# Optimization experiments

Hardware: AMD Instinct MI355X
Metric: run time of the kernel (lower is better)

## Reference

```python
import jax, jax.numpy as jnp
import numpy as np

C = 64            # in_channels
IC = C // 2       # inter_channels (channel_rate=2)
R = 16            # reduction_ratio
EPS = 1e-5


def setup_inputs() -> dict:
    key = jax.random.key(0)
    ks = jax.random.split(key, 16)
    s = 0.05
    return {
        "x": jax.random.normal(ks[0], (16, C, 64, 25), dtype=jnp.float32),
        # 1x1 conv projections (common_v, key, query): [out, in] + bias
        "Wv": jax.random.normal(ks[1], (IC, C), dtype=jnp.float32) * s,
        "bv": jax.random.normal(ks[2], (IC,), dtype=jnp.float32) * s,
        "Wk": jax.random.normal(ks[3], (IC, C), dtype=jnp.float32) * s,
        "bk": jax.random.normal(ks[4], (IC,), dtype=jnp.float32) * s,
        "Wq": jax.random.normal(ks[5], (IC, C), dtype=jnp.float32) * s,
        "bq": jax.random.normal(ks[6], (IC,), dtype=jnp.float32) * s,
        # Trans_s: conv1x1 back to C + BatchNorm2d params (nonzero so output is non-trivial)
        "Wt": jax.random.normal(ks[7], (C, IC), dtype=jnp.float32) * s,
        "bt": jax.random.normal(ks[8], (C,), dtype=jnp.float32) * s,
        "gamma": jax.random.normal(ks[9], (C,), dtype=jnp.float32) * 0.5 + 1.0,
        "beta": jax.random.normal(ks[10], (C,), dtype=jnp.float32) * s,
        # ChannelGate MLP: Linear(C, C//R), Linear(C//R, C)
        "W1": jax.random.normal(ks[11], (C // R, C), dtype=jnp.float32) * s,
        "b1": jax.random.normal(ks[12], (C // R,), dtype=jnp.float32) * s,
        "W2": jax.random.normal(ks[13], (C, C // R), dtype=jnp.float32) * s,
        "b2": jax.random.normal(ks[14], (C,), dtype=jnp.float32) * s,
    }


def _conv1x1(x, W, b):
    # x: [N, Cin, T, V]; W: [Cout, Cin]
    return jnp.einsum('nctv,oc->notv', x, W) + b[None, :, None, None]


def reference(x, Wv, bv, Wk, bk, Wq, bq, Wt, bt, gamma, beta, W1, b1, W2, b2):
    N, Cc, T, V = x.shape
    TV = T * V
    ic = Wv.shape[0]

    v_x = _conv1x1(x, Wv, bv).reshape(N, ic, TV).transpose(0, 2, 1)  # [N, TV, ic]
    k_x = _conv1x1(x, Wk, bk).reshape(N, ic, TV).transpose(0, 2, 1)  # [N, TV, ic]
    q_x = _conv1x1(x, Wq, bq).reshape(N, ic, TV)                      # [N, ic, TV]

    # Unscaled dot-product attention over TV tokens (full [N, TV, TV] matrix)
    A = jnp.einsum('nti,nis->nts', k_x, q_x)
    attn = jax.nn.softmax(A, axis=-1)
    p = jnp.einsum('nts,nsi->nti', attn, v_x)                         # [N, TV, ic]
    p = p.transpose(0, 2, 1).reshape(N, ic, T, V)

    # Trans_s: conv1x1 + BatchNorm2d (training-mode batch statistics)
    p = _conv1x1(p, Wt, bt)
    mean = p.mean(axis=(0, 2, 3), keepdims=True)
    var = p.var(axis=(0, 2, 3), keepdims=True)
    p = (p - mean) * jax.lax.rsqrt(var + EPS)
    p = p * gamma[None, :, None, None] + beta[None, :, None, None]

    # ChannelGate (avg pool only) applied to original x
    avg = x.mean(axis=(2, 3))                                          # [N, C]
    h = jax.nn.relu(avg @ W1.T + b1)
    gate = jax.nn.sigmoid(h @ W2.T + b2)                               # [N, C]

    return gate[:, :, None, None] * p + x
```

## Files before the change

kernel.cpp:

```cpp
#include <hip/hip_runtime.h>
#include <hip/hip_bf16.h>
#include <math.h>

#define NB   16
#define CC   64
#define ICH  32
#define TV   1600
#define NTV  (NB*TV)

typedef __bf16 bf16x8 __attribute__((ext_vector_type(8)));
typedef float  f32x4  __attribute__((ext_vector_type(4)));

__global__ __launch_bounds__(256) void proj_gate_kernel(
    const float* __restrict__ x,
    const float* __restrict__ Wv, const float* __restrict__ bv,
    const float* __restrict__ Wk, const float* __restrict__ bk,
    const float* __restrict__ Wq, const float* __restrict__ bq,
    __bf16* __restrict__ Qb, __bf16* __restrict__ Kb,
    __bf16* __restrict__ VTb, float* __restrict__ AVG) {
  if (blockIdx.x >= 400) {
    int b = blockIdx.x - 400;
    int n = b >> 2, cq = b & 3;
    int c16 = threadIdx.x >> 4, l = threadIdx.x & 15;
    int c = cq * 16 + c16;
    const float4* xp = (const float4*)(x + ((size_t)n * CC + c) * TV) + l;
    float s = 0.f;
#pragma unroll
    for (int i = 0; i < 25; ++i) {
      float4 v = xp[i * 16];
      s += v.x + v.y + v.z + v.w;
    }
#pragma unroll
    for (int off = 8; off >= 1; off >>= 1) s += __shfl_down(s, off, 16);
    if (l == 0) AVG[n * CC + c] = s * (1.0f / (float)TV);
    return;
  }

  int tile = blockIdx.x >> 2;
  int og   = blockIdx.x & 3;
  int ob = og * 8;
  int tvIdx = tile * 256 + threadIdx.x;
  int n = tvIdx / TV, tv = tvIdx % TV;

  float av[8], ak[8], aq[8];
#pragma unroll
  for (int j = 0; j < 8; ++j) { av[j] = bv[ob+j]; ak[j] = bk[ob+j]; aq[j] = bq[ob+j]; }

  const float* xp = x + (size_t)n * CC * TV + tv;
#pragma unroll 8
  for (int c = 0; c < CC; ++c) {
    float xc = xp[c * TV];
#pragma unroll
    for (int j = 0; j < 8; ++j) {
      av[j] = fmaf(Wv[(ob + j) * CC + c], xc, av[j]);
      ak[j] = fmaf(Wk[(ob + j) * CC + c], xc, ak[j]);
      aq[j] = fmaf(Wq[(ob + j) * CC + c], xc, aq[j]);
    }
  }

  bf16x8 t;
#pragma unroll
  for (int j = 0; j < 8; ++j) t[j] = (__bf16)ak[j];
  int base = (n * TV + tv) * ICH + ob;
  *(bf16x8*)(Qb + base) = t;
#pragma unroll
  for (int j = 0; j < 8; ++j) t[j] = (__bf16)aq[j];
  *(bf16x8*)(Kb + base) = t;
#pragma unroll
  for (int j = 0; j < 8; ++j)
    VTb[(n * ICH + ob + j) * TV + tv] = (__bf16)av[j];
}

__global__ __launch_bounds__(256) void attn_kernel(
    const __bf16* __restrict__ Qb, const __bf16* __restrict__ Kb,
    const __bf16* __restrict__ VTb, float* __restrict__ P) {
  __shared__ __bf16 lds[4 * 4608];
  int b = blockIdx.x;
  int r8 = b & 7, qq = b >> 3;
  int n = r8 * 2 + (qq >= 50 ? 1 : 0);
  int rowTile = (qq >= 50) ? qq - 50 : qq;
  int row0 = rowTile * 32;

  int w = threadIdx.x >> 6;
  int lane = threadIdx.x & 63;
  int m = lane & 15, q = lane >> 4;

  __bf16* Pw = lds + w * 4608;

  const __bf16* Qn = Qb  + (size_t)n * TV * ICH;
  const __bf16* Kn = Kb  + (size_t)n * TV * ICH;
  const __bf16* Vn = VTb + (size_t)n * ICH * TV;

  bf16x8 aQ0 = *(const bf16x8*)(Qn + (row0 + m) * ICH + q * 8);
  bf16x8 aQ1 = *(const bf16x8*)(Qn + (row0 + 16 + m) * ICH + q * 8);

  f32x4 o00 = {0.f,0.f,0.f,0.f}, o01 = {0.f,0.f,0.f,0.f};
  f32x4 o10 = {0.f,0.f,0.f,0.f}, o11 = {0.f,0.f,0.f,0.f};
  f32x4 ls0 = {0.f,0.f,0.f,0.f}, ls1 = {0.f,0.f,0.f,0.f};
  const f32x4 zero = {0.f,0.f,0.f,0.f};

  int nch = (w == 3) ? 7 : 6;

  for (int jj = 0; jj < nch; jj += 2) {
    int sA = (4 * jj + (3 - w)) * 64;
    bool hasB = (jj + 1) < nch;
    int sB = hasB ? (4 * (jj + 1) + (3 - w)) * 64 : sA;

#pragma unroll
    for (int st = 0; st < 4; ++st) {
      bf16x8 bK = *(const bf16x8*)(Kn + (sA + st * 16 + m) * ICH + q * 8);
      f32x4 a0 = __builtin_amdgcn_mfma_f32_16x16x32_bf16(aQ0, bK, zero, 0, 0, 0);
      f32x4 a1 = __builtin_amdgcn_mfma_f32_16x16x32_bf16(aQ1, bK, zero, 0, 0, 0);
#pragma unroll
      for (int r = 0; r < 4; ++r) {
        float e0 = __expf(a0[r]); ls0[r] += e0;
        float e1 = __expf(a1[r]); ls1[r] += e1;
        Pw[(q * 4 + r) * 72 + st * 16 + m]        = (__bf16)e0;
        Pw[1152 + (q * 4 + r) * 72 + st * 16 + m] = (__bf16)e1;
      }
    }
    if (hasB) {
#pragma unroll
      for (int st = 0; st < 4; ++st) {
        bf16x8 bK = *(const bf16x8*)(Kn + (sB + st * 16 + m) * ICH + q * 8);
        f32x4 a0 = __builtin_amdgcn_mfma_f32_16x16x32_bf16(aQ0, bK, zero, 0, 0, 0);
        f32x4 a1 = __builtin_amdgcn_mfma_f32_16x16x32_bf16(aQ1, bK, zero, 0, 0, 0);
#pragma unroll
        for (int r = 0; r < 4; ++r) {
          float e0 = __expf(a0[r]); ls0[r] += e0;
          float e1 = __expf(a1[r]); ls1[r] += e1;
          Pw[2304 + (q * 4 + r) * 72 + st * 16 + m] = (__bf16)e0;
          Pw[3456 + (q * 4 + r) * 72 + st * 16 + m] = (__bf16)e1;
        }
      }
    }
    asm volatile("s_waitcnt lgkmcnt(0)" ::: "memory");
#pragma unroll
    for (int kc = 0; kc < 2; ++kc) {
      bf16x8 aP0 = *(const bf16x8*)(Pw + m * 72 + kc * 32 + q * 8);
      bf16x8 aP1 = *(const bf16x8*)(Pw + 1152 + m * 72 + kc * 32 + q * 8);
#pragma unroll
      for (int ict = 0; ict < 2; ++ict) {
        bf16x8 bV = *(const bf16x8*)(Vn + (ict * 16 + m) * TV + sA + kc * 32 + q * 8);
        if (ict == 0) {
          o00 = __builtin_amdgcn_mfma_f32_16x16x32_bf16(aP0, bV, o00, 0, 0, 0);
          o10 = __builtin_amdgcn_mfma_f32_16x16x32_bf16(aP1, bV, o10, 0, 0, 0);
        } else {
          o01 = __builtin_amdgcn_mfma_f32_16x16x32_bf16(aP0, bV, o01, 0, 0, 0);
          o11 = __builtin_amdgcn_mfma_f32_16x16x32_bf16(aP1, bV, o11, 0, 0, 0);
        }
      }
    }
    if (hasB) {
#pragma unroll
      for (int kc = 0; kc < 2; ++kc) {
        bf16x8 aP0 = *(const bf16x8*)(Pw + 2304 + m * 72 + kc * 32 + q * 8);
        bf16x8 aP1 = *(const bf16x8*)(Pw + 3456 + m * 72 + kc * 32 + q * 8);
#pragma unroll
        for (int ict = 0; ict < 2; ++ict) {
          bf16x8 bV = *(const bf16x8*)(Vn + (ict * 16 + m) * TV + sB + kc * 32 + q * 8);
          if (ict == 0) {
            o00 = __builtin_amdgcn_mfma_f32_16x16x32_bf16(aP0, bV, o00, 0, 0, 0);
            o10 = __builtin_amdgcn_mfma_f32_16x16x32_bf16(aP1, bV, o10, 0, 0, 0);
          } else {
            o01 = __builtin_amdgcn_mfma_f32_16x16x32_bf16(aP0, bV, o01, 0, 0, 0);
            o11 = __builtin_amdgcn_mfma_f32_16x16x32_bf16(aP1, bV, o11, 0, 0, 0);
          }
        }
      }
    }
  }

#pragma unroll
  for (int mask = 1; mask <= 8; mask <<= 1) {
#pragma unroll
    for (int r = 0; r < 4; ++r) {
      ls0[r] += __shfl_xor(ls0[r], mask, 64);
      ls1[r] += __shfl_xor(ls1[r], mask, 64);
    }
  }

  __syncthreads();
  float* mf = (float*)lds;
  float* mp = mf + (w * 64 + lane) * 24;
#pragma unroll
  for (int r = 0; r < 4; ++r) {
    mp[r]      = o00[r]; mp[4 + r]  = o01[r];
    mp[8 + r]  = o10[r]; mp[12 + r] = o11[r];
    mp[16 + r] = ls0[r]; mp[20 + r] = ls1[r];
  }
  __syncthreads();
  if (w == 0) {
#pragma unroll
    for (int ww = 1; ww < 4; ++ww) {
      const float* sp = mf + (ww * 64 + lane) * 24;
#pragma unroll
      for (int r = 0; r < 4; ++r) {
        o00[r] += sp[r];      o01[r] += sp[4 + r];
        o10[r] += sp[8 + r];  o11[r] += sp[12 + r];
        ls0[r] += sp[16 + r]; ls1[r] += sp[20 + r];
      }
    }
#pragma unroll
    for (int r = 0; r < 4; ++r) {
      float i0 = 1.f / ls0[r], i1 = 1.f / ls1[r];
      int pb0 = (n * TV + row0 + q * 4 + r) * ICH;
      int pb1 = pb0 + 16 * ICH;
      P[pb0 + m]      = o00[r] * i0;
      P[pb0 + 16 + m] = o01[r] * i0;
      P[pb1 + m]      = o10[r] * i1;
      P[pb1 + 16 + m] = o11[r] * i1;
    }
  }
}

__global__ __launch_bounds__(256) void stats_kernel(
    const float* __restrict__ P, const float* __restrict__ Wt,
    const float* __restrict__ bt, float* __restrict__ PS2) {
  int cg = blockIdx.x / 100;
  int tb = blockIdx.x % 100;
  int tvIdx = tb * 256 + threadIdx.x;
  int n = tvIdx / TV, tv = tvIdx % TV;

  union { f32x4 v[8]; float f[32]; } p;
  const f32x4* pp = (const f32x4*)(P + ((size_t)(n * TV + tv)) * ICH);
#pragma unroll
  for (int u = 0; u < 8; ++u) p.v[u] = pp[u];

  __shared__ float red[2][4][8];
  int w = threadIdx.x >> 6, lane = threadIdx.x & 63;
#pragma unroll
  for (int j = 0; j < 8; ++j) {
    int c = cg * 8 + j;
    float y = bt[c];
#pragma unroll
    for (int i = 0; i < ICH; ++i) y = fmaf(Wt[c * ICH + i], p.f[i], y);
    float y2 = y * y;
#pragma unroll
    for (int off = 32; off >= 1; off >>= 1) {
      y  += __shfl_xor(y,  off, 64);
      y2 += __shfl_xor(y2, off, 64);
    }
    if (lane == 0) { red[0][w][j] = y; red[1][w][j] = y2; }
  }
  __syncthreads();
  if (threadIdx.x < 16) {
    int which = threadIdx.x >> 3, j = threadIdx.x & 7;
    float s = red[which][0][j] + red[which][1][j] +
              red[which][2][j] + red[which][3][j];
    PS2[blockIdx.x * 16 + which * 8 + j] = s;
  }
}

__global__ __launch_bounds__(128) void finalize_stats(
    const float* __restrict__ PS2, const float* __restrict__ gamma,
    const float* __restrict__ beta, const float* __restrict__ AVG,
    const float* __restrict__ W1, const float* __restrict__ b1,
    const float* __restrict__ W2, const float* __restrict__ b2,
    float* __restrict__ SS, float* __restrict__ GATE) {
  int t = threadIdx.x;
  __shared__ float sh[NB][4];
  if (t < 64) {
    int c = t, cg = c >> 3, j = c & 7;
    float s = 0.f, ss = 0.f;
    for (int b = 0; b < 100; ++b) {
      int base = (cg * 100 + b) * 16;
      s  += PS2[base + j];
      ss += PS2[base + 8 + j];
    }
    float mean = s * (1.f / (float)NTV);
    float var  = ss * (1.f / (float)NTV) - mean * mean;
    float scale = rsqrtf(var + 1e-5f) * gamma[c];
    SS[c] = scale;
    SS[64 + c] = beta[c] - mean * scale;
    int n = t >> 2, jj = t & 3;
    float h = b1[jj];
    for (int c2 = 0; c2 < CC; ++c2)
      h = fmaf(W1[jj * CC + c2], AVG[n * CC + c2], h);
    sh[n][jj] = fmaxf(h, 0.f);
  }
  __syncthreads();
#pragma unroll
  for (int u = 0; u < 8; ++u) {
    int idx = t * 8 + u;
    int n = idx >> 6, c = idx & 63;
    float g = b2[c];
#pragma unroll
    for (int jj = 0; jj < 4; ++jj) g = fmaf(W2[c * 4 + jj], sh[n][jj], g);
    GATE[idx] = 1.f / (1.f + __expf(-g));
  }
}

__global__ __launch_bounds__(256) void apply_kernel(
    const float* __restrict__ P, const float* __restrict__ Wt,
    const float* __restrict__ bt, const float* __restrict__ SS,
    const float* __restrict__ gate, const float* __restrict__ x,
    float* __restrict__ out) {
  int cg = blockIdx.x / 100;
  int tb = blockIdx.x % 100;
  int tvIdx = tb * 256 + threadIdx.x;
  int n = tvIdx / TV, tv = tvIdx % TV;

  union { f32x4 v[8]; float f[32]; } p;
  const f32x4* pp = (const f32x4*)(P + ((size_t)(n * TV + tv)) * ICH);
#pragma unroll
  for (int u = 0; u < 8; ++u) p.v[u] = pp[u];

#pragma unroll
  for (int j = 0; j < 8; ++j) {
    int c = cg * 8 + j;
    float y = bt[c];
#pragma unroll
    for (int i = 0; i < ICH; ++i) y = fmaf(Wt[c * ICH + i], p.f[i], y);
    size_t idx = ((size_t)(n * CC + c)) * TV + tv;
    out[idx] = gate[n * CC + c] * fmaf(y, SS[c], SS[64 + c]) + x[idx];
  }
}

extern "C" void kernel_launch(void* const* d_in, const int* in_sizes, int n_in,
                              void* d_out, int out_size, void* d_ws, size_t ws_size,
                              hipStream_t stream) {
  const float* x     = (const float*)d_in[0];
  const float* Wv    = (const float*)d_in[1];
  const float* bv    = (const float*)d_in[2];
  const float* Wk    = (const float*)d_in[3];
  const float* bk    = (const float*)d_in[4];
  const float* Wq    = (const float*)d_in[5];
  const float* bq    = (const float*)d_in[6];
  const float* Wt    = (const float*)d_in[7];
  const float* bt    = (const float*)d_in[8];
  const float* gamma = (const float*)d_in[9];
  const float* beta  = (const float*)d_in[10];
  const float* W1    = (const float*)d_in[11];
  const float* b1    = (const float*)d_in[12];
  const float* W2    = (const float*)d_in[13];
  const float* b2    = (const float*)d_in[14];
  float* out = (float*)d_out;
  char* ws = (char*)d_ws;

  const size_t E = 819200;
  __bf16* Qb  = (__bf16*)(ws);
  __bf16* Kb  = (__bf16*)(ws + 2*E);
  __bf16* VTb = (__bf16*)(ws + 4*E);
  float*  P   = (float*) (ws + 6*E);
  float*  PS2 = (float*) (ws + 10*E);
  float*  SS  = (float*) (ws + 10*E + 51200);
  float*  GATE= (float*) (ws + 10*E + 51712);
  float*  AVG = out;

  proj_gate_kernel<<<464, 256, 0, stream>>>(x, Wv, bv, Wk, bk, Wq, bq,
                                            Qb, Kb, VTb, AVG);
  attn_kernel<<<NB * 50, 256, 0, stream>>>(Qb, Kb, VTb, P);
  stats_kernel<<<800, 256, 0, stream>>>(P, Wt, bt, PS2);
  finalize_stats<<<1, 128, 0, stream>>>(PS2, gamma, beta, AVG,
                                        W1, b1, W2, b2, SS, GATE);
  apply_kernel<<<800, 256, 0, stream>>>(P, Wt, bt, SS, GATE, x, out);
}
```

Baseline: 157.4 us.

## Fuse BN statistics into attention epilogue, store P as bf16, split projection blocks

Removes the separate stats kernel: the attention kernel now stages its normalized output tile in LDS, computes the Trans_s conv per channel and accumulates sum and sum-of-squares into a global buffer with atomics, which the projection kernel zeroes. The P intermediate is written in bf16 to halve its traffic, and the apply kernel reads and widens it. The projection kernel is split into three times as many blocks, each computing one of V/K/Q, to raise parallelism at the cost of re-reading x. Risks include lower precision in P for the apply step and atomic accumulation order nondeterminism.

```diff
diff --git a/kernel.cpp b/kernel.cpp
--- a/kernel.cpp
+++ b/kernel.cpp
@@ -17,9 +17,14 @@
     const float* __restrict__ Wk, const float* __restrict__ bk,
     const float* __restrict__ Wq, const float* __restrict__ bq,
     __bf16* __restrict__ Qb, __bf16* __restrict__ Kb,
-    __bf16* __restrict__ VTb, float* __restrict__ AVG) {
-  if (blockIdx.x >= 400) {
-    int b = blockIdx.x - 400;
+    __bf16* __restrict__ VTb, float* __restrict__ AVG,
+    float* __restrict__ GS) {
+  if (blockIdx.x == 1264) {
+    if (threadIdx.x < 128) GS[threadIdx.x] = 0.f;
+    return;
+  }
+  if (blockIdx.x >= 1200) {
+    int b = blockIdx.x - 1200;
     int n = b >> 2, cq = b & 3;
     int c16 = threadIdx.x >> 4, l = threadIdx.x & 15;
     int c = cq * 16 + c16;
@@ -36,44 +41,50 @@
     return;
   }
 
-  int tile = blockIdx.x >> 2;
-  int og   = blockIdx.x & 3;
+  int tile = blockIdx.x / 12;
+  int sub  = blockIdx.x % 12;
+  int p = sub >> 2, og = sub & 3;
   int ob = og * 8;
   int tvIdx = tile * 256 + threadIdx.x;
   int n = tvIdx / TV, tv = tvIdx % TV;
 
-  float av[8], ak[8], aq[8];
-#pragma unroll
-  for (int j = 0; j < 8; ++j) { av[j] = bv[ob+j]; ak[j] = bk[ob+j]; aq[j] = bq[ob+j]; }
+  const float* W; const float* B;
+  if (p == 0)      { W = Wv; B = bv; }
+  else if (p == 1) { W = Wk; B = bk; }
+  else             { W = Wq; B = bq; }
+
+  float acc[8];
+#pragma unroll
+  for (int j = 0; j < 8; ++j) acc[j] = B[ob + j];
 
   const float* xp = x + (size_t)n * CC * TV + tv;
-#pragma unroll 8
+#pragma unroll 16
   for (int c = 0; c < CC; ++c) {
     float xc = xp[c * TV];
 #pragma unroll
-    for (int j = 0; j < 8; ++j) {
-      av[j] = fmaf(Wv[(ob + j) * CC + c], xc, av[j]);
-      ak[j] = fmaf(Wk[(ob + j) * CC + c], xc, ak[j]);
-      aq[j] = fmaf(Wq[(ob + j) * CC + c], xc, aq[j]);
-    }
-  }
-
-  bf16x8 t;
-#pragma unroll
-  for (int j = 0; j < 8; ++j) t[j] = (__bf16)ak[j];
-  int base = (n * TV + tv) * ICH + ob;
-  *(bf16x8*)(Qb + base) = t;
-#pragma unroll
-  for (int j = 0; j < 8; ++j) t[j] = (__bf16)aq[j];
-  *(bf16x8*)(Kb + base) = t;
-#pragma unroll
-  for (int j = 0; j < 8; ++j)
-    VTb[(n * ICH + ob + j) * TV + tv] = (__bf16)av[j];
+    for (int j = 0; j < 8; ++j)
+      acc[j] = fmaf(W[(ob + j) * CC + c], xc, acc[j]);
+  }
+
+  if (p == 0) {
+#pragma unroll
+    for (int j = 0; j < 8; ++j)
+      VTb[(n * ICH + ob + j) * TV + tv] = (__bf16)acc[j];
+  } else {
+    bf16x8 t;
+#pragma unroll
+    for (int j = 0; j < 8; ++j) t[j] = (__bf16)acc[j];
+    int base = (n * TV + tv) * ICH + ob;
+    if (p == 1) *(bf16x8*)(Qb + base) = t;
+    else        *(bf16x8*)(Kb + base) = t;
+  }
 }
 
 __global__ __launch_bounds__(256) void attn_kernel(
     const __bf16* __restrict__ Qb, const __bf16* __restrict__ Kb,
-    const __bf16* __restrict__ VTb, float* __restrict__ P) {
+    const __bf16* __restrict__ VTb, __bf16* __restrict__ P,
+    const float* __restrict__ Wt, const float* __restrict__ bt,
+    float* __restrict__ GS) {
   __shared__ __bf16 lds[4 * 4608];
   int b = blockIdx.x;
   int r8 = b & 7, qq = b >> 3;
@@ -180,8 +191,11 @@
     }
   }
 
-  __syncthreads();
   float* mf = (float*)lds;
+  float* Pl = mf + 6144;
+  float* red = mf + 7424;
+
+  __syncthreads();
   float* mp = mf + (w * 64 + lane) * 24;
 #pragma unroll
   for (int r = 0; r < 4; ++r) {
@@ -204,56 +218,49 @@
 #pragma unroll
     for (int r = 0; r < 4; ++r) {
       float i0 = 1.f / ls0[r], i1 = 1.f / ls1[r];
+      float p00 = o00[r] * i0, p01 = o01[r] * i0;
+      float p10 = o10[r] * i1, p11 = o11[r] * i1;
       int pb0 = (n * TV + row0 + q * 4 + r) * ICH;
       int pb1 = pb0 + 16 * ICH;
-      P[pb0 + m]      = o00[r] * i0;
-      P[pb0 + 16 + m] = o01[r] * i0;
-      P[pb1 + m]      = o10[r] * i1;
-      P[pb1 + 16 + m] = o11[r] * i1;
-    }
-  }
-}
-
-__global__ __launch_bounds__(256) void stats_kernel(
-    const float* __restrict__ P, const float* __restrict__ Wt,
-    const float* __restrict__ bt, float* __restrict__ PS2) {
-  int cg = blockIdx.x / 100;
-  int tb = blockIdx.x % 100;
-  int tvIdx = tb * 256 + threadIdx.x;
-  int n = tvIdx / TV, tv = tvIdx % TV;
-
-  union { f32x4 v[8]; float f[32]; } p;
-  const f32x4* pp = (const f32x4*)(P + ((size_t)(n * TV + tv)) * ICH);
-#pragma unroll
-  for (int u = 0; u < 8; ++u) p.v[u] = pp[u];
-
-  __shared__ float red[2][4][8];
-  int w = threadIdx.x >> 6, lane = threadIdx.x & 63;
-#pragma unroll
-  for (int j = 0; j < 8; ++j) {
-    int c = cg * 8 + j;
-    float y = bt[c];
-#pragma unroll
-    for (int i = 0; i < ICH; ++i) y = fmaf(Wt[c * ICH + i], p.f[i], y);
-    float y2 = y * y;
-#pragma unroll
-    for (int off = 32; off >= 1; off >>= 1) {
-      y  += __shfl_xor(y,  off, 64);
-      y2 += __shfl_xor(y2, off, 64);
-    }
-    if (lane == 0) { red[0][w][j] = y; red[1][w][j] = y2; }
-  }
-  __syncthreads();
-  if (threadIdx.x < 16) {
-    int which = threadIdx.x >> 3, j = threadIdx.x & 7;
-    float s = red[which][0][j] + red[which][1][j] +
-              red[which][2][j] + red[which][3][j];
-    PS2[blockIdx.x * 16 + which * 8 + j] = s;
+      P[pb0 + m]      = (__bf16)p00;
+      P[pb0 + 16 + m] = (__bf16)p01;
+      P[pb1 + m]      = (__bf16)p10;
+      P[pb1 + 16 + m] = (__bf16)p11;
+      Pl[(q * 4 + r) * 33 + m]           = p00;
+      Pl[(q * 4 + r) * 33 + 16 + m]      = p01;
+      Pl[(16 + q * 4 + r) * 33 + m]      = p10;
+      Pl[(16 + q * 4 + r) * 33 + 16 + m] = p11;
+    }
+  }
+  __syncthreads();
+
+  int c = threadIdx.x & 63;
+  float wr[ICH];
+#pragma unroll
+  for (int i = 0; i < ICH; ++i) wr[i] = Wt[c * ICH + i];
+  float bc = bt[c];
+  float sy = 0.f, sy2 = 0.f;
+#pragma unroll
+  for (int rr = 0; rr < 8; ++rr) {
+    const float* pr = Pl + (w * 8 + rr) * 33;
+    float y = bc;
+#pragma unroll
+    for (int i = 0; i < ICH; ++i) y = fmaf(wr[i], pr[i], y);
+    sy += y; sy2 += y * y;
+  }
+  red[w * 128 + c]      = sy;
+  red[w * 128 + 64 + c] = sy2;
+  __syncthreads();
+  if (threadIdx.x < 128) {
+    int which = threadIdx.x >> 6, cc = threadIdx.x & 63;
+    float s = red[which * 64 + cc]       + red[128 + which * 64 + cc] +
+              red[256 + which * 64 + cc] + red[384 + which * 64 + cc];
+    atomicAdd(GS + which * 64 + cc, s);
   }
 }
 
 __global__ __launch_bounds__(128) void finalize_stats(
-    const float* __restrict__ PS2, const float* __restrict__ gamma,
+    const float* __restrict__ GS, const float* __restrict__ gamma,
     const float* __restrict__ beta, const float* __restrict__ AVG,
     const float* __restrict__ W1, const float* __restrict__ b1,
     const float* __restrict__ W2, const float* __restrict__ b2,
@@ -261,15 +268,9 @@
   int t = threadIdx.x;
   __shared__ float sh[NB][4];
   if (t < 64) {
-    int c = t, cg = c >> 3, j = c & 7;
-    float s = 0.f, ss = 0.f;
-    for (int b = 0; b < 100; ++b) {
-      int base = (cg * 100 + b) * 16;
-      s  += PS2[base + j];
-      ss += PS2[base + 8 + j];
-    }
-    float mean = s * (1.f / (float)NTV);
-    float var  = ss * (1.f / (float)NTV) - mean * mean;
+    int c = t;
+    float mean = GS[c] * (1.f / (float)NTV);
+    float var  = GS[64 + c] * (1.f / (float)NTV) - mean * mean;
     float scale = rsqrtf(var + 1e-5f) * gamma[c];
     SS[c] = scale;
     SS[64 + c] = beta[c] - mean * scale;
@@ -292,7 +293,7 @@
 }
 
 __global__ __launch_bounds__(256) void apply_kernel(
-    const float* __restrict__ P, const float* __restrict__ Wt,
+    const __bf16* __restrict__ P, const float* __restrict__ Wt,
     const float* __restrict__ bt, const float* __restrict__ SS,
     const float* __restrict__ gate, const float* __restrict__ x,
     float* __restrict__ out) {
@@ -301,17 +302,21 @@
   int tvIdx = tb * 256 + threadIdx.x;
   int n = tvIdx / TV, tv = tvIdx % TV;
 
-  union { f32x4 v[8]; float f[32]; } p;
-  const f32x4* pp = (const f32x4*)(P + ((size_t)(n * TV + tv)) * ICH);
-#pragma unroll
-  for (int u = 0; u < 8; ++u) p.v[u] = pp[u];
+  float f[ICH];
+  const bf16x8* pp = (const bf16x8*)(P + ((size_t)(n * TV + tv)) * ICH);
+#pragma unroll
+  for (int u = 0; u < 4; ++u) {
+    bf16x8 v = pp[u];
+#pragma unroll
+    for (int j = 0; j < 8; ++j) f[u * 8 + j] = (float)v[j];
+  }
 
 #pragma unroll
   for (int j = 0; j < 8; ++j) {
     int c = cg * 8 + j;
     float y = bt[c];
 #pragma unroll
-    for (int i = 0; i < ICH; ++i) y = fmaf(Wt[c * ICH + i], p.f[i], y);
+    for (int i = 0; i < ICH; ++i) y = fmaf(Wt[c * ICH + i], f[i], y);
     size_t idx = ((size_t)(n * CC + c)) * TV + tv;
     out[idx] = gate[n * CC + c] * fmaf(y, SS[c], SS[64 + c]) + x[idx];
   }
@@ -342,17 +347,16 @@
   __bf16* Qb  = (__bf16*)(ws);
   __bf16* Kb  = (__bf16*)(ws + 2*E);
   __bf16* VTb = (__bf16*)(ws + 4*E);
-  float*  P   = (float*) (ws + 6*E);
-  float*  PS2 = (float*) (ws + 10*E);
-  float*  SS  = (float*) (ws + 10*E + 51200);
-  float*  GATE= (float*) (ws + 10*E + 51712);
+  __bf16* Pb  = (__bf16*)(ws + 6*E);
+  float*  GS  = (float*) (ws + 8*E);
+  float*  SS  = (float*) (ws + 8*E + 512);
+  float*  GATE= (float*) (ws + 8*E + 1024);
   float*  AVG = out;
 
-  proj_gate_kernel<<<464, 256, 0, stream>>>(x, Wv, bv, Wk, bk, Wq, bq,
-                                            Qb, Kb, VTb, AVG);
-  attn_kernel<<<NB * 50, 256, 0, stream>>>(Qb, Kb, VTb, P);
-  stats_kernel<<<800, 256, 0, stream>>>(P, Wt, bt, PS2);
-  finalize_stats<<<1, 128, 0, stream>>>(PS2, gamma, beta, AVG,
+  proj_gate_kernel<<<1265, 256, 0, stream>>>(x, Wv, bv, Wk, bk, Wq, bq,
+                                             Qb, Kb, VTb, AVG, GS);
+  attn_kernel<<<NB * 50, 256, 0, stream>>>(Qb, Kb, VTb, Pb, Wt, bt, GS);
+  finalize_stats<<<1, 128, 0, stream>>>(GS, gamma, beta, AVG,
                                         W1, b1, W2, b2, SS, GATE);
-  apply_kernel<<<800, 256, 0, stream>>>(P, Wt, bt, SS, GATE, x, out);
-}
+  apply_kernel<<<800, 256, 0, stream>>>(Pb, Wt, bt, SS, GATE, x, out);
+}
```

Measured after the change: 153.6 us. 1.02x faster.
